# Kernel tuning notes

Measured on AMD Instinct MI355X. Metric: run time of the kernel, lower is better.

The kernel has to match this reference:

```python
import jax, jax.numpy as jnp
import numpy as np

NHID = 512
PROJ = 64          # fixed 64-dim projection from the source code
N_NODES = 16384
N_CLAIM = 4096
N_EVID = 8192
N_GRAPHS = 64


def setup_inputs() -> dict:
    key = jax.random.key(0)
    ks = jax.random.split(key, 10)
    x = jax.random.normal(ks[0], (N_NODES, NHID), dtype=jnp.float32)
    batch = jnp.sort(jax.random.randint(ks[1], (N_NODES,), 0, N_GRAPHS, dtype=jnp.int64))
    claim_index = jax.random.randint(ks[2], (N_CLAIM,), 0, N_NODES, dtype=jnp.int64)
    evidence_index = jax.random.randint(ks[3], (N_EVID,), 0, N_NODES, dtype=jnp.int64)
    # Linear params (PyTorch Linear: y = x @ W.T + b; store as [in, out] here)
    s_c = 1.0 / np.sqrt(NHID)
    Wc = jax.random.uniform(ks[4], (NHID, PROJ), jnp.float32, -s_c, s_c)
    bc = jax.random.uniform(ks[5], (PROJ,), jnp.float32, -s_c, s_c)
    We = jax.random.uniform(ks[6], (NHID, PROJ), jnp.float32, -s_c, s_c)
    be = jax.random.uniform(ks[7], (PROJ,), jnp.float32, -s_c, s_c)
    s_a = 1.0 / np.sqrt(4 * NHID)
    Wa = jax.random.uniform(ks[8], (4 * NHID, NHID), jnp.float32, -s_a, s_a)
    ba = jax.random.uniform(ks[9], (NHID,), jnp.float32, -s_a, s_a)
    return {"x": x, "batch": batch, "claim_index": claim_index,
            "evidence_index": evidence_index,
            "Wc": Wc, "bc": bc, "We": We, "be": be, "Wa": Wa, "ba": ba}


def reference(x, batch, claim_index, evidence_index, Wc, bc, We, be, Wa, ba):
    claim_batch = batch[claim_index]          # [Nc]
    evidence_batch = batch[evidence_index]    # [Ne]
    # block-diagonal mask: 0 where same graph, -inf otherwise
    same = claim_batch[:, None] == evidence_batch[None, :]
    mask = jnp.where(same, 0.0, -jnp.inf).astype(jnp.float32)  # [Nc, Ne]

    claim = x[claim_index]       # [Nc, nhid]
    evidence = x[evidence_index]  # [Ne, nhid]

    weight_c = claim @ Wc + bc    # [Nc, 64]
    weight_e = evidence @ We + be  # [Ne, 64]
    scores = weight_c @ weight_e.T + mask          # [Nc, Ne]
    attn = jax.nn.softmax(scores, axis=-1)
    claim_new = attn @ evidence                    # [Nc, nhid]

    a = jnp.concatenate([claim, claim_new, claim - claim_new, claim * claim_new], axis=-1)
    a = a @ Wa + ba               # [Nc, nhid]

    # global_mean_pool over claim_batch
    seg_sum = jax.ops.segment_sum(a, claim_batch, num_segments=N_GRAPHS)
    counts = jax.ops.segment_sum(jnp.ones((a.shape[0],), a.dtype), claim_batch,
                                 num_segments=N_GRAPHS)
    res = seg_sum / jnp.maximum(counts, 1.0)[:, None]  # [B, nhid]
    return res
```

## Files before the change

kernel.cpp:

```cpp
#include <hip/hip_runtime.h>
#include <hip/hip_bf16.h>

#define NHID 512
#define PROJ 64
#define NC 4096
#define NEV 8192
#define NG 64
#define NCMAX 128
#define NE_CAP 256
#define DSLICES 4
#define DW 128

typedef __attribute__((ext_vector_type(8))) short s16x8;
typedef __attribute__((ext_vector_type(8))) unsigned short u16x8;
typedef __attribute__((ext_vector_type(4))) float f32x4;

#define P_S_STRIDE 264
#define P_S_BYTES  (NCMAX * P_S_STRIDE * 2)
#define REGB_OFF   P_S_BYTES
#define WE_S_STRIDE 72
#define WC_S_OFF   (REGB_OFF + NE_CAP * WE_S_STRIDE * 2)
#define CN_S_STRIDE 132
#define MISC_OFF   (REGB_OFF + P_S_BYTES)
#define SMEM_BYTES (MISC_OFF + 1536)

static __device__ __forceinline__ unsigned short f2b(float f) {
  union { __hip_bfloat16 h; unsigned short u; } v;
  v.h = __float2bfloat16(f);
  return v.u;
}

template <int NPT>
__device__ __forceinline__ void compact_pairs(
    const int* __restrict__ batch, const int* __restrict__ idx, int g,
    int* __restrict__ off_out, int* __restrict__ cnt_out, int2* __restrict__ pairs) {
  __shared__ int wtot[4], wless[4];
  int t = threadIdx.x, lane = t & 63, w = t >> 6;
  int vals[NPT], nid[NPT];
  int base_i = t * NPT;
  int eq = 0, less = 0;
#pragma unroll
  for (int j = 0; j < NPT; j++) {
    int node = idx[base_i + j];
    int v = batch[node];
    vals[j] = v;
    nid[j] = node;
    eq += (v == g) ? 1 : 0;
    less += (v < g) ? 1 : 0;
  }
  int s = eq;
#pragma unroll
  for (int off = 1; off < 64; off <<= 1) {
    int o = __shfl_up(s, off);
    if (lane >= off) s += o;
  }
  int ls = less;
#pragma unroll
  for (int off = 32; off; off >>= 1) ls += __shfl_xor(ls, off);
  if (lane == 63) wtot[w] = s;
  if (lane == 0) wless[w] = ls;
  __syncthreads();
  int wbase = 0;
#pragma unroll
  for (int k = 0; k < 4; k++)
    if (k < w) wbase += wtot[k];
  int base = wless[0] + wless[1] + wless[2] + wless[3];
  int pos = base + wbase + (s - eq);
#pragma unroll
  for (int j = 0; j < NPT; j++) {
    if (vals[j] == g) pairs[pos++] = make_int2(base_i + j, nid[j]);
  }
  if (t == 255) {
    cnt_out[g] = wbase + s;
    off_out[g] = base;
  }
}

__global__ __launch_bounds__(256) void k_front(
    const float* __restrict__ Wc, const float* __restrict__ We,
    unsigned short* __restrict__ WcT, unsigned short* __restrict__ WeT,
    const int* __restrict__ batch, const int* __restrict__ cidx,
    const int* __restrict__ eidx, int* __restrict__ c_off, int* __restrict__ c_cnt,
    int2* __restrict__ c_pair, int* __restrict__ e_off, int* __restrict__ e_cnt,
    int2* __restrict__ e_pair) {
  int b = blockIdx.x;
  if (b < 16) {
    __shared__ float ts[64][65];
    const float* src = (b < 8) ? Wc : We;
    unsigned short* dst = (b < 8) ? WcT : WeT;
    int k0 = (b & 7) * 64;
    int t = threadIdx.x;
    int c = t & 63, r0 = t >> 6;
#pragma unroll
    for (int p = 0; p < 16; p++) {
      int r = r0 * 16 + p;
      ts[r][c] = src[(size_t)(k0 + r) * 64 + c];
    }
    __syncthreads();
    int n = t >> 2, q = t & 3;
    unsigned short tmp[16];
#pragma unroll
    for (int j = 0; j < 16; j++) tmp[j] = f2b(ts[q * 16 + j][n]);
    u16x8* dp = (u16x8*)(dst + (size_t)n * NHID + k0 + q * 16);
    dp[0] = *(u16x8*)tmp;
    dp[1] = *(u16x8*)(tmp + 8);
  } else if (b < 80) {
    compact_pairs<NC / 256>(batch, cidx, b - 16, c_off, c_cnt, c_pair);
  } else {
    compact_pairs<NEV / 256>(batch, eidx, b - 80, e_off, e_cnt, e_pair);
  }
}

__global__ __launch_bounds__(256) void k_proj(
    const float* __restrict__ x, const int* __restrict__ cidx,
    const int* __restrict__ eidx, const unsigned short* __restrict__ WcT,
    const unsigned short* __restrict__ WeT, const float* __restrict__ bc,
    const float* __restrict__ be, const float* __restrict__ Wa,
    unsigned short* __restrict__ WaT, unsigned short* __restrict__ wcp,
    unsigned short* __restrict__ wep) {
  __shared__ __align__(16) char sm[64 * 65 * 4];
  int b = blockIdx.x;
  int t = threadIdx.x;
  if (b >= 768) {
    int tb = b - 768;
    float(*ts)[65] = (float(*)[65])sm;
    int k0 = (tb >> 3) * 64, n0 = (tb & 7) * 64;
    int c = t & 63, r0 = t >> 6;
#pragma unroll
    for (int p = 0; p < 16; p++) {
      int r = r0 * 16 + p;
      ts[r][c] = Wa[(size_t)(k0 + r) * NHID + n0 + c];
    }
    __syncthreads();
    int n = t >> 2, q = t & 3;
    unsigned short tmp[16];
#pragma unroll
    for (int j = 0; j < 16; j++) tmp[j] = f2b(ts[q * 16 + j][n]);
    u16x8* dp = (u16x8*)(WaT + (size_t)(n0 + n) * (4 * NHID) + k0 + q * 16);
    dp[0] = *(u16x8*)tmp;
    dp[1] = *(u16x8*)(tmp + 8);
    return;
  }
  float(*red)[16][64] = (float(*)[16][64])sm;
  const int* idx; const unsigned short* WT; const float* bias;
  unsigned short* out; int base;
  if (b < NC / 16) { idx = cidx; WT = WcT; bias = bc; out = wcp; base = b * 16; }
  else             { idx = eidx; WT = WeT; bias = be; out = wep; base = (b - NC / 16) * 16; }
  int lane = t & 63, kh = t >> 6;
  int ln = lane & 15, kb = lane >> 4;
  const float* xr = x + (size_t)idx[base + ln] * NHID + kh * 128;
  const unsigned short* wb = WT + kh * 128;
  f32x4 acc[4];
#pragma unroll
  for (int nt = 0; nt < 4; nt++) acc[nt] = (f32x4){0.f, 0.f, 0.f, 0.f};
#pragma unroll
  for (int kt = 0; kt < 4; kt++) {
    int k0 = kt * 32 + kb * 8;
    float4 p0 = *(const float4*)(xr + k0);
    float4 p1 = *(const float4*)(xr + k0 + 4);
    s16x8 a;
    a[0] = (short)f2b(p0.x); a[1] = (short)f2b(p0.y);
    a[2] = (short)f2b(p0.z); a[3] = (short)f2b(p0.w);
    a[4] = (short)f2b(p1.x); a[5] = (short)f2b(p1.y);
    a[6] = (short)f2b(p1.z); a[7] = (short)f2b(p1.w);
#pragma unroll
    for (int nt = 0; nt < 4; nt++) {
      s16x8 bf = *(const s16x8*)(wb + (size_t)(nt * 16 + ln) * NHID + k0);
      acc[nt] = __builtin_amdgcn_mfma_f32_16x16x32_bf16(a, bf, acc[nt], 0, 0, 0);
    }
  }
#pragma unroll
  for (int nt = 0; nt < 4; nt++)
#pragma unroll
    for (int r = 0; r < 4; r++)
      red[kh][kb * 4 + r][nt * 16 + ln] = acc[nt][r];
  __syncthreads();
  for (int i = t; i < 512; i += 256) {
    int row = i >> 5, cp = i & 31;
    int c0 = cp * 2;
    float v0 = red[0][row][c0] + red[1][row][c0] + red[2][row][c0] + red[3][row][c0] + bias[c0];
    float v1 = red[0][row][c0 + 1] + red[1][row][c0 + 1] + red[2][row][c0 + 1] + red[3][row][c0 + 1] + bias[c0 + 1];
    unsigned int pk = (unsigned)f2b(v0) | ((unsigned)f2b(v1) << 16);
    *(unsigned int*)(out + (size_t)(base + row) * PROJ + c0) = pk;
  }
}

__global__ __launch_bounds__(512, 2) void k_attn(
    const float* __restrict__ x, const unsigned short* __restrict__ wcp,
    const unsigned short* __restrict__ wep, const int* __restrict__ c_off,
    const int* __restrict__ c_cnt, const int2* __restrict__ c_pair,
    const int* __restrict__ e_off, const int* __restrict__ e_cnt,
    const int2* __restrict__ e_pair, unsigned short* __restrict__ mcb) {
  __shared__ __align__(16) char smem[SMEM_BYTES];
  unsigned short* P_s  = (unsigned short*)(smem);
  unsigned short* we_s = (unsigned short*)(smem + REGB_OFF);
  unsigned short* wc_s = (unsigned short*)(smem + WC_S_OFF);
  unsigned short* evT  = (unsigned short*)(smem + REGB_OFF);
  unsigned int*   evT32 = (unsigned int*)(smem + REGB_OFF);
  float*          cn_s = (float*)(smem + REGB_OFF);
  float*          pp   = (float*)(smem);
  int* ev_id = (int*)(smem + MISC_OFF);
  int* cl_id = (int*)(smem + MISC_OFF + 1024);

  int g = blockIdx.x >> 2;
  int ds = blockIdx.x & 3;
  int dsbase = ds * DW;
  int t = threadIdx.x, lane = t & 63, w = t >> 6;
  int ln = lane & 15, kb = lane >> 4;

  int ne = min(e_cnt[g], NE_CAP);
  int eoff = e_off[g];
  int ccnt_full = c_cnt[g];
  int nloc = min(ccnt_full, NCMAX);
  int coff = c_off[g];
  if (nloc <= 0) {
    int q = t >> 7, d = t & 127;
    mcb[(size_t)g * 4 * NHID + q * NHID + dsbase + d] = 0;
    return;
  }
  int KT = (ne + 31) >> 5;
  int NT = KT * 2;

  for (int e = t; e < NE_CAP; e += 512)
    ev_id[e] = (e < ne) ? e_pair[eoff + e].y : 0;
  if (t < NCMAX) cl_id[t] = (t < nloc) ? c_pair[coff + t].y : 0;
  {
    int q = t & 7, er = t >> 3;
    for (int base_ = 0; base_ < NE_CAP; base_ += 64) {
      int e = base_ + er;
      u16x8 v = (u16x8){0, 0, 0, 0, 0, 0, 0, 0};
      if (e < ne) v = *(const u16x8*)(wep + (size_t)e_pair[eoff + e].x * PROJ + q * 8);
      *(u16x8*)(we_s + e * WE_S_STRIDE + q * 8) = v;
    }
    for (int base_ = 0; base_ < NCMAX; base_ += 64) {
      int c = base_ + er;
      u16x8 v = (u16x8){0, 0, 0, 0, 0, 0, 0, 0};
      if (c < nloc) v = *(const u16x8*)(wcp + (size_t)c_pair[coff + c].x * PROJ + q * 8);
      *(u16x8*)(wc_s + c * WE_S_STRIDE + q * 8) = v;
    }
  }
  __syncthreads();

  float4 eva[8], evb[8];
#pragma unroll
  for (int it = 0; it < 8; it++) {
    int idx2 = it * 512 + t;
    int ep = idx2 & 127;
    int dq = idx2 >> 7;
    int d0 = dq * 4;
    int e0 = ep * 2;
    eva[it] = make_float4(0.f, 0.f, 0.f, 0.f);
    evb[it] = make_float4(0.f, 0.f, 0.f, 0.f);
    if (e0 < ne)     eva[it] = *(const float4*)(x + (size_t)ev_id[e0] * NHID + dsbase + d0);
    if (e0 + 1 < ne) evb[it] = *(const float4*)(x + (size_t)ev_id[e0 + 1] * NHID + dsbase + d0);
  }

  {
    f32x4 sa[16];
#pragma unroll
    for (int i = 0; i < 16; i++) sa[i] = (f32x4){0.f, 0.f, 0.f, 0.f};
    const unsigned short* arow = wc_s + ((w << 4) + ln) * WE_S_STRIDE;
#pragma unroll
    for (int ks = 0; ks < 2; ks++) {
      s16x8 af = *(const s16x8*)(arow + ks * 32 + kb * 8);
#pragma unroll
      for (int nt = 0; nt < 16; nt++) {
        if (nt < NT) {
          s16x8 bf = *(const s16x8*)(we_s + (nt * 16 + ln) * WE_S_STRIDE + ks * 32 + kb * 8);
          sa[nt] = __builtin_amdgcn_mfma_f32_16x16x32_bf16(af, bf, sa[nt], 0, 0, 0);
        }
      }
    }
#pragma unroll
    for (int r = 0; r < 4; r++) {
      int claim = (w << 4) + (kb << 2) + r;
      float mx = -1e30f;
#pragma unroll
      for (int nt = 0; nt < 16; nt++) {
        if (nt < NT) {
          float v = sa[nt][r];
          v = (nt * 16 + ln < ne) ? v : -1e30f;
          sa[nt][r] = v;
          mx = fmaxf(mx, v);
        }
      }
      mx = fmaxf(mx, __shfl_xor(mx, 1));
      mx = fmaxf(mx, __shfl_xor(mx, 2));
      mx = fmaxf(mx, __shfl_xor(mx, 4));
      mx = fmaxf(mx, __shfl_xor(mx, 8));
      float sum = 0.f;
#pragma unroll
      for (int nt = 0; nt < 16; nt++) {
        if (nt < NT) {
          float p = __expf(sa[nt][r] - mx);
          sa[nt][r] = p;
          sum += p;
        }
      }
      sum += __shfl_xor(sum, 1);
      sum += __shfl_xor(sum, 2);
      sum += __shfl_xor(sum, 4);
      sum += __shfl_xor(sum, 8);
      float inv = 1.f / sum;
#pragma unroll
      for (int nt = 0; nt < 16; nt++) {
        if (nt < NT)
          P_s[claim * P_S_STRIDE + nt * 16 + ln] = f2b(sa[nt][r] * inv);
      }
    }
  }
  __syncthreads();

#pragma unroll
  for (int it = 0; it < 8; it++) {
    int idx2 = it * 512 + t;
    int ep = idx2 & 127;
    int dq = idx2 >> 7;
    int d0 = dq * 4;
    float4 va = eva[it], vb = evb[it];
    evT32[(d0 + 0) * (P_S_STRIDE / 2) + ep] = (unsigned)f2b(va.x) | ((unsigned)f2b(vb.x) << 16);
    evT32[(d0 + 1) * (P_S_STRIDE / 2) + ep] = (unsigned)f2b(va.y) | ((unsigned)f2b(vb.y) << 16);
    evT32[(d0 + 2) * (P_S_STRIDE / 2) + ep] = (unsigned)f2b(va.z) | ((unsigned)f2b(vb.z) << 16);
    evT32[(d0 + 3) * (P_S_STRIDE / 2) + ep] = (unsigned)f2b(va.w) | ((unsigned)f2b(vb.w) << 16);
  }
  __syncthreads();

  int dq4 = (t & 31) * 4;
  int mg = t >> 5;
  float4 cl_r[8];
#pragma unroll
  for (int mi = 0; mi < 8; mi++) {
    int m = mg + mi * 16;
    cl_r[mi] = make_float4(0.f, 0.f, 0.f, 0.f);
    if (m < nloc)
      cl_r[mi] = *(const float4*)(x + (size_t)cl_id[m] * NHID + dsbase + dq4);
  }

  int mw = w >> 1, nw = w & 1;
  int m0 = mw * 32, n0 = nw * 64;
  f32x4 pc[8];
#pragma unroll
  for (int i = 0; i < 8; i++) pc[i] = (f32x4){0.f, 0.f, 0.f, 0.f};
  {
    const unsigned short* prow0 = P_s + (m0 + ln) * P_S_STRIDE + kb * 8;
    const unsigned short* prow1 = prow0 + 16 * P_S_STRIDE;
#pragma unroll
    for (int kt = 0; kt < 8; kt++) {
      if (kt < KT) {
        int k0 = kt * 32;
        s16x8 a0 = *(const s16x8*)(prow0 + k0);
        s16x8 a1 = *(const s16x8*)(prow1 + k0);
#pragma unroll
        for (int nt = 0; nt < 4; nt++) {
          s16x8 bf = *(const s16x8*)(evT + (n0 + nt * 16 + ln) * P_S_STRIDE + k0 + kb * 8);
          pc[nt]     = __builtin_amdgcn_mfma_f32_16x16x32_bf16(a0, bf, pc[nt], 0, 0, 0);
          pc[4 + nt] = __builtin_amdgcn_mfma_f32_16x16x32_bf16(a1, bf, pc[4 + nt], 0, 0, 0);
        }
      }
    }
  }
  __syncthreads();

#pragma unroll
  for (int mi = 0; mi < 2; mi++) {
#pragma unroll
    for (int nt = 0; nt < 4; nt++) {
      f32x4 v = pc[mi * 4 + nt];
#pragma unroll
      for (int r = 0; r < 4; r++)
        cn_s[(m0 + mi * 16 + (kb << 2) + r) * CN_S_STRIDE + n0 + nt * 16 + ln] = v[r];
    }
  }
  __syncthreads();

  {
    float4 scl = make_float4(0.f, 0.f, 0.f, 0.f);
    float4 scn = make_float4(0.f, 0.f, 0.f, 0.f);
    float4 spr = make_float4(0.f, 0.f, 0.f, 0.f);
#pragma unroll
    for (int mi = 0; mi < 8; mi++) {
      int m = mg + mi * 16;
      if (m < nloc) {
        float4 cl = cl_r[mi];
        float4 cn = *(const float4*)(cn_s + m * CN_S_STRIDE + dq4);
        scl.x += cl.x; scl.y += cl.y; scl.z += cl.z; scl.w += cl.w;
        scn.x += cn.x; scn.y += cn.y; scn.z += cn.z; scn.w += cn.w;
        spr.x += cl.x * cn.x; spr.y += cl.y * cn.y;
        spr.z += cl.z * cn.z; spr.w += cl.w * cn.w;
      }
    }
    *(float4*)(pp + mg * 128 + dq4) = scl;
    *(float4*)(pp + 2048 + mg * 128 + dq4) = scn;
    *(float4*)(pp + 4096 + mg * 128 + dq4) = spr;
  }
  __syncthreads();

  {
    int q = t >> 7, d = t & 127;
    float inv = 1.f / (float)max(ccnt_full, 1);
    float v = 0.f;
    if (q == 0) {
#pragma unroll
      for (int mg2 = 0; mg2 < 16; mg2++) v += pp[mg2 * 128 + d];
    } else if (q == 1) {
#pragma unroll
      for (int mg2 = 0; mg2 < 16; mg2++) v += pp[2048 + mg2 * 128 + d];
    } else if (q == 2) {
#pragma unroll
      for (int mg2 = 0; mg2 < 16; mg2++) v += pp[mg2 * 128 + d] - pp[2048 + mg2 * 128 + d];
    } else {
#pragma unroll
      for (int mg2 = 0; mg2 < 16; mg2++) v += pp[4096 + mg2 * 128 + d];
    }
    mcb[(size_t)g * 4 * NHID + q * NHID + dsbase + d] = f2b(v * inv);
  }
}

__global__ __launch_bounds__(512) void k_out(
    const unsigned short* __restrict__ mc, const unsigned short* __restrict__ WaT,
    const float* __restrict__ ba, float* __restrict__ out) {
  __shared__ float red[2][64][16];
  int n0 = blockIdx.x * 16;
  int t = threadIdx.x, lane = t & 63, wv = t >> 6;
  int mh = wv & 3, kh = wv >> 2;
  int ln = lane & 15, kb = lane >> 4;
  f32x4 acc = (f32x4){0.f, 0.f, 0.f, 0.f};
  const unsigned short* arow = mc + (size_t)(mh * 16 + ln) * (4 * NHID) + kh * 1024;
  const unsigned short* wcol = WaT + (size_t)(n0 + ln) * (4 * NHID) + kh * 1024;
#pragma unroll 4
  for (int kt = 0; kt < 32; kt++) {
    int k0 = kt * 32 + kb * 8;
    s16x8 af = *(const s16x8*)(arow + k0);
    s16x8 bf = *(const s16x8*)(wcol + k0);
    acc = __builtin_amdgcn_mfma_f32_16x16x32_bf16(af, bf, acc, 0, 0, 0);
  }
#pragma unroll
  for (int r = 0; r < 4; r++)
    red[kh][mh * 16 + kb * 4 + r][ln] = acc[r];
  __syncthreads();
  for (int i = t; i < 1024; i += 512) {
    int row = i >> 4, col = i & 15;
    out[(size_t)row * NHID + n0 + col] = red[0][row][col] + red[1][row][col] + ba[n0 + col];
  }
}

extern "C" void kernel_launch(void* const* d_in, const int* in_sizes, int n_in,
                              void* d_out, int out_size, void* d_ws, size_t ws_size,
                              hipStream_t stream) {
  const float* x = (const float*)d_in[0];
  const int* batch = (const int*)d_in[1];
  const int* cidx = (const int*)d_in[2];
  const int* eidx = (const int*)d_in[3];
  const float* Wc = (const float*)d_in[4];
  const float* bc = (const float*)d_in[5];
  const float* We = (const float*)d_in[6];
  const float* be = (const float*)d_in[7];
  const float* Wa = (const float*)d_in[8];
  const float* ba = (const float*)d_in[9];
  float* out = (float*)d_out;

  char* w = (char*)d_ws;
  int* c_off = (int*)w;    w += NG * 4;
  int* c_cnt = (int*)w;    w += NG * 4;
  int* e_off = (int*)w;    w += NG * 4;
  int* e_cnt = (int*)w;    w += NG * 4;
  int2* c_pair = (int2*)w; w += (size_t)NC * 8;
  int2* e_pair = (int2*)w; w += (size_t)NEV * 8;
  unsigned short* wcp = (unsigned short*)w; w += (size_t)NC * PROJ * 2;
  unsigned short* wep = (unsigned short*)w; w += (size_t)NEV * PROJ * 2;
  unsigned short* WcT = (unsigned short*)w; w += (size_t)PROJ * NHID * 2;
  unsigned short* WeT = (unsigned short*)w; w += (size_t)PROJ * NHID * 2;
  unsigned short* WaT = (unsigned short*)w; w += (size_t)NHID * 4 * NHID * 2;
  unsigned short* mcb = (unsigned short*)w; w += (size_t)NG * 4 * NHID * 2;

  k_front<<<144, 256, 0, stream>>>(Wc, We, WcT, WeT, batch, cidx, eidx,
                                   c_off, c_cnt, c_pair, e_off, e_cnt, e_pair);
  k_proj<<<768 + 256, 256, 0, stream>>>(x, cidx, eidx, WcT, WeT, bc, be, Wa, WaT,
                                        wcp, wep);
  k_attn<<<NG * DSLICES, 512, 0, stream>>>(x, wcp, wep, c_off, c_cnt, c_pair,
                                           e_off, e_cnt, e_pair, mcb);
  k_out<<<32, 512, 0, stream>>>(mcb, WaT, ba, out);
}
```

Baseline: 58.30 us.

## Split attention kernel into per-graph score kernel and per-slice PV kernel

The fused attention kernel is split in two. A per-graph kernel computes the softmax probabilities once and writes them to a global bf16 buffer. A separate PV kernel, run per d-slice, reads those probabilities from global memory, so the score GEMM and softmax are no longer repeated for each of the four d-slices. The PV kernel uses less LDS, targets higher occupancy, and drops the cn_s staging buffer by reducing claim statistics with shuffles. In exchange it adds a kernel launch, a global round trip for the probabilities, and scalar rather than vectorized gathers of claim rows.

```diff
diff --git a/kernel.cpp b/kernel.cpp
--- a/kernel.cpp
+++ b/kernel.cpp
@@ -10,19 +10,13 @@
 #define NE_CAP 256
 #define DSLICES 4
 #define DW 128
+#define WE_S_STRIDE 72
+#define EV_STRIDE 264
+#define PG_STRIDE 256
 
 typedef __attribute__((ext_vector_type(8))) short s16x8;
 typedef __attribute__((ext_vector_type(8))) unsigned short u16x8;
 typedef __attribute__((ext_vector_type(4))) float f32x4;
-
-#define P_S_STRIDE 264
-#define P_S_BYTES  (NCMAX * P_S_STRIDE * 2)
-#define REGB_OFF   P_S_BYTES
-#define WE_S_STRIDE 72
-#define WC_S_OFF   (REGB_OFF + NE_CAP * WE_S_STRIDE * 2)
-#define CN_S_STRIDE 132
-#define MISC_OFF   (REGB_OFF + P_S_BYTES)
-#define SMEM_BYTES (MISC_OFF + 1536)
 
 static __device__ __forceinline__ unsigned short f2b(float f) {
   union { __hip_bfloat16 h; unsigned short u; } v;
@@ -185,22 +179,107 @@
   }
 }
 
-__global__ __launch_bounds__(512, 2) void k_attn(
-    const float* __restrict__ x, const unsigned short* __restrict__ wcp,
-    const unsigned short* __restrict__ wep, const int* __restrict__ c_off,
-    const int* __restrict__ c_cnt, const int2* __restrict__ c_pair,
-    const int* __restrict__ e_off, const int* __restrict__ e_cnt,
-    const int2* __restrict__ e_pair, unsigned short* __restrict__ mcb) {
-  __shared__ __align__(16) char smem[SMEM_BYTES];
-  unsigned short* P_s  = (unsigned short*)(smem);
-  unsigned short* we_s = (unsigned short*)(smem + REGB_OFF);
-  unsigned short* wc_s = (unsigned short*)(smem + WC_S_OFF);
-  unsigned short* evT  = (unsigned short*)(smem + REGB_OFF);
-  unsigned int*   evT32 = (unsigned int*)(smem + REGB_OFF);
-  float*          cn_s = (float*)(smem + REGB_OFF);
-  float*          pp   = (float*)(smem);
-  int* ev_id = (int*)(smem + MISC_OFF);
-  int* cl_id = (int*)(smem + MISC_OFF + 1024);
+__global__ __launch_bounds__(512) void k_score(
+    const unsigned short* __restrict__ wcp, const unsigned short* __restrict__ wep,
+    const int* __restrict__ c_off, const int* __restrict__ c_cnt,
+    const int2* __restrict__ c_pair, const int* __restrict__ e_off,
+    const int* __restrict__ e_cnt, const int2* __restrict__ e_pair,
+    unsigned short* __restrict__ P_g) {
+  __shared__ __align__(16) unsigned short we_s[NE_CAP * WE_S_STRIDE];
+  __shared__ __align__(16) unsigned short wc_s[NCMAX * WE_S_STRIDE];
+  int g = blockIdx.x;
+  int t = threadIdx.x, lane = t & 63, w = t >> 6;
+  int ln = lane & 15, kb = lane >> 4;
+  int ne = min(e_cnt[g], NE_CAP);
+  int eoff = e_off[g];
+  int nloc = min(c_cnt[g], NCMAX);
+  int coff = c_off[g];
+  if (nloc <= 0) return;
+  int KT = (ne + 31) >> 5;
+  int NT = KT * 2;
+  {
+    int q = t & 7, er = t >> 3;
+    for (int base_ = 0; base_ < NE_CAP; base_ += 64) {
+      int e = base_ + er;
+      u16x8 v = (u16x8){0, 0, 0, 0, 0, 0, 0, 0};
+      if (e < ne) v = *(const u16x8*)(wep + (size_t)e_pair[eoff + e].x * PROJ + q * 8);
+      *(u16x8*)(we_s + e * WE_S_STRIDE + q * 8) = v;
+    }
+    for (int base_ = 0; base_ < NCMAX; base_ += 64) {
+      int c = base_ + er;
+      u16x8 v = (u16x8){0, 0, 0, 0, 0, 0, 0, 0};
+      if (c < nloc) v = *(const u16x8*)(wcp + (size_t)c_pair[coff + c].x * PROJ + q * 8);
+      *(u16x8*)(wc_s + c * WE_S_STRIDE + q * 8) = v;
+    }
+  }
+  __syncthreads();
+  f32x4 sa[16];
+#pragma unroll
+  for (int i = 0; i < 16; i++) sa[i] = (f32x4){0.f, 0.f, 0.f, 0.f};
+  const unsigned short* arow = wc_s + ((w << 4) + ln) * WE_S_STRIDE;
+#pragma unroll
+  for (int ks = 0; ks < 2; ks++) {
+    s16x8 af = *(const s16x8*)(arow + ks * 32 + kb * 8);
+#pragma unroll
+    for (int nt = 0; nt < 16; nt++) {
+      if (nt < NT) {
+        s16x8 bf = *(const s16x8*)(we_s + (nt * 16 + ln) * WE_S_STRIDE + ks * 32 + kb * 8);
+        sa[nt] = __builtin_amdgcn_mfma_f32_16x16x32_bf16(af, bf, sa[nt], 0, 0, 0);
+      }
+    }
+  }
+#pragma unroll
+  for (int r = 0; r < 4; r++) {
+    int claim = (w << 4) + (kb << 2) + r;
+    float mx = -1e30f;
+#pragma unroll
+    for (int nt = 0; nt < 16; nt++) {
+      if (nt < NT) {
+        float v = sa[nt][r];
+        v = (nt * 16 + ln < ne) ? v : -1e30f;
+        sa[nt][r] = v;
+        mx = fmaxf(mx, v);
+      }
+    }
+    mx = fmaxf(mx, __shfl_xor(mx, 1));
+    mx = fmaxf(mx, __shfl_xor(mx, 2));
+    mx = fmaxf(mx, __shfl_xor(mx, 4));
+    mx = fmaxf(mx, __shfl_xor(mx, 8));
+    float sum = 0.f;
+#pragma unroll
+    for (int nt = 0; nt < 16; nt++) {
+      if (nt < NT) {
+        float p = __expf(sa[nt][r] - mx);
+        sa[nt][r] = p;
+        sum += p;
+      }
+    }
+    sum += __shfl_xor(sum, 1);
+    sum += __shfl_xor(sum, 2);
+    sum += __shfl_xor(sum, 4);
+    sum += __shfl_xor(sum, 8);
+    float inv = 1.f / sum;
+    if (claim < nloc) {
+      unsigned short* prow = P_g + (size_t)(coff + claim) * PG_STRIDE;
+#pragma unroll
+      for (int nt = 0; nt < 16; nt++) {
+        if (nt < NT) prow[nt * 16 + ln] = f2b(sa[nt][r] * inv);
+      }
+    }
+  }
+}
+
+__global__ __launch_bounds__(512, 4) void k_pv(
+    const float* __restrict__ x, const unsigned short* __restrict__ P_g,
+    const int* __restrict__ c_off, const int* __restrict__ c_cnt,
+    const int2* __restrict__ c_pair, const int* __restrict__ e_off,
+    const int* __restrict__ e_cnt, const int2* __restrict__ e_pair,
+    unsigned short* __restrict__ mcb) {
+  __shared__ __align__(16) unsigned short evT[DW * EV_STRIDE];
+  __shared__ float pp[4][3][DW];
+  __shared__ int ev_id[NE_CAP];
+  __shared__ int cl_id[NCMAX];
+  unsigned int* evT32 = (unsigned int*)evT;
 
   int g = blockIdx.x >> 2;
   int ds = blockIdx.x & 3;
@@ -219,29 +298,12 @@
     return;
   }
   int KT = (ne + 31) >> 5;
-  int NT = KT * 2;
 
   for (int e = t; e < NE_CAP; e += 512)
     ev_id[e] = (e < ne) ? e_pair[eoff + e].y : 0;
   if (t < NCMAX) cl_id[t] = (t < nloc) ? c_pair[coff + t].y : 0;
-  {
-    int q = t & 7, er = t >> 3;
-    for (int base_ = 0; base_ < NE_CAP; base_ += 64) {
-      int e = base_ + er;
-      u16x8 v = (u16x8){0, 0, 0, 0, 0, 0, 0, 0};
-      if (e < ne) v = *(const u16x8*)(wep + (size_t)e_pair[eoff + e].x * PROJ + q * 8);
-      *(u16x8*)(we_s + e * WE_S_STRIDE + q * 8) = v;
-    }
-    for (int base_ = 0; base_ < NCMAX; base_ += 64) {
-      int c = base_ + er;
-      u16x8 v = (u16x8){0, 0, 0, 0, 0, 0, 0, 0};
-      if (c < nloc) v = *(const u16x8*)(wcp + (size_t)c_pair[coff + c].x * PROJ + q * 8);
-      *(u16x8*)(wc_s + c * WE_S_STRIDE + q * 8) = v;
-    }
-  }
-  __syncthreads();
-
-  float4 eva[8], evb[8];
+  __syncthreads();
+
 #pragma unroll
   for (int it = 0; it < 8; it++) {
     int idx2 = it * 512 + t;
@@ -249,92 +311,16 @@
     int dq = idx2 >> 7;
     int d0 = dq * 4;
     int e0 = ep * 2;
-    eva[it] = make_float4(0.f, 0.f, 0.f, 0.f);
-    evb[it] = make_float4(0.f, 0.f, 0.f, 0.f);
-    if (e0 < ne)     eva[it] = *(const float4*)(x + (size_t)ev_id[e0] * NHID + dsbase + d0);
-    if (e0 + 1 < ne) evb[it] = *(const float4*)(x + (size_t)ev_id[e0 + 1] * NHID + dsbase + d0);
-  }
-
-  {
-    f32x4 sa[16];
-#pragma unroll
-    for (int i = 0; i < 16; i++) sa[i] = (f32x4){0.f, 0.f, 0.f, 0.f};
-    const unsigned short* arow = wc_s + ((w << 4) + ln) * WE_S_STRIDE;
-#pragma unroll
-    for (int ks = 0; ks < 2; ks++) {
-      s16x8 af = *(const s16x8*)(arow + ks * 32 + kb * 8);
-#pragma unroll
-      for (int nt = 0; nt < 16; nt++) {
-        if (nt < NT) {
-          s16x8 bf = *(const s16x8*)(we_s + (nt * 16 + ln) * WE_S_STRIDE + ks * 32 + kb * 8);
-          sa[nt] = __builtin_amdgcn_mfma_f32_16x16x32_bf16(af, bf, sa[nt], 0, 0, 0);
-        }
-      }
-    }
-#pragma unroll
-    for (int r = 0; r < 4; r++) {
-      int claim = (w << 4) + (kb << 2) + r;
-      float mx = -1e30f;
-#pragma unroll
-      for (int nt = 0; nt < 16; nt++) {
-        if (nt < NT) {
-          float v = sa[nt][r];
-          v = (nt * 16 + ln < ne) ? v : -1e30f;
-          sa[nt][r] = v;
-          mx = fmaxf(mx, v);
-        }
-      }
-      mx = fmaxf(mx, __shfl_xor(mx, 1));
-      mx = fmaxf(mx, __shfl_xor(mx, 2));
-      mx = fmaxf(mx, __shfl_xor(mx, 4));
-      mx = fmaxf(mx, __shfl_xor(mx, 8));
-      float sum = 0.f;
-#pragma unroll
-      for (int nt = 0; nt < 16; nt++) {
-        if (nt < NT) {
-          float p = __expf(sa[nt][r] - mx);
-          sa[nt][r] = p;
-          sum += p;
-        }
-      }
-      sum += __shfl_xor(sum, 1);
-      sum += __shfl_xor(sum, 2);
-      sum += __shfl_xor(sum, 4);
-      sum += __shfl_xor(sum, 8);
-      float inv = 1.f / sum;
-#pragma unroll
-      for (int nt = 0; nt < 16; nt++) {
-        if (nt < NT)
-          P_s[claim * P_S_STRIDE + nt * 16 + ln] = f2b(sa[nt][r] * inv);
-      }
-    }
-  }
-  __syncthreads();
-
-#pragma unroll
-  for (int it = 0; it < 8; it++) {
-    int idx2 = it * 512 + t;
-    int ep = idx2 & 127;
-    int dq = idx2 >> 7;
-    int d0 = dq * 4;
-    float4 va = eva[it], vb = evb[it];
-    evT32[(d0 + 0) * (P_S_STRIDE / 2) + ep] = (unsigned)f2b(va.x) | ((unsigned)f2b(vb.x) << 16);
-    evT32[(d0 + 1) * (P_S_STRIDE / 2) + ep] = (unsigned)f2b(va.y) | ((unsigned)f2b(vb.y) << 16);
-    evT32[(d0 + 2) * (P_S_STRIDE / 2) + ep] = (unsigned)f2b(va.z) | ((unsigned)f2b(vb.z) << 16);
-    evT32[(d0 + 3) * (P_S_STRIDE / 2) + ep] = (unsigned)f2b(va.w) | ((unsigned)f2b(vb.w) << 16);
-  }
-  __syncthreads();
-
-  int dq4 = (t & 31) * 4;
-  int mg = t >> 5;
-  float4 cl_r[8];
-#pragma unroll
-  for (int mi = 0; mi < 8; mi++) {
-    int m = mg + mi * 16;
-    cl_r[mi] = make_float4(0.f, 0.f, 0.f, 0.f);
-    if (m < nloc)
-      cl_r[mi] = *(const float4*)(x + (size_t)cl_id[m] * NHID + dsbase + dq4);
-  }
+    float4 va = make_float4(0.f, 0.f, 0.f, 0.f);
+    float4 vb = make_float4(0.f, 0.f, 0.f, 0.f);
+    if (e0 < ne)     va = *(const float4*)(x + (size_t)ev_id[e0] * NHID + dsbase + d0);
+    if (e0 + 1 < ne) vb = *(const float4*)(x + (size_t)ev_id[e0 + 1] * NHID + dsbase + d0);
+    evT32[(d0 + 0) * (EV_STRIDE / 2) + ep] = (unsigned)f2b(va.x) | ((unsigned)f2b(vb.x) << 16);
+    evT32[(d0 + 1) * (EV_STRIDE / 2) + ep] = (unsigned)f2b(va.y) | ((unsigned)f2b(vb.y) << 16);
+    evT32[(d0 + 2) * (EV_STRIDE / 2) + ep] = (unsigned)f2b(va.z) | ((unsigned)f2b(vb.z) << 16);
+    evT32[(d0 + 3) * (EV_STRIDE / 2) + ep] = (unsigned)f2b(va.w) | ((unsigned)f2b(vb.w) << 16);
+  }
+  __syncthreads();
 
   int mw = w >> 1, nw = w & 1;
   int m0 = mw * 32, n0 = nw * 64;
@@ -342,8 +328,8 @@
 #pragma unroll
   for (int i = 0; i < 8; i++) pc[i] = (f32x4){0.f, 0.f, 0.f, 0.f};
   {
-    const unsigned short* prow0 = P_s + (m0 + ln) * P_S_STRIDE + kb * 8;
-    const unsigned short* prow1 = prow0 + 16 * P_S_STRIDE;
+    const unsigned short* prow0 = P_g + (size_t)(coff + m0 + ln) * PG_STRIDE + kb * 8;
+    const unsigned short* prow1 = prow0 + 16 * PG_STRIDE;
 #pragma unroll
     for (int kt = 0; kt < 8; kt++) {
       if (kt < KT) {
@@ -352,65 +338,56 @@
         s16x8 a1 = *(const s16x8*)(prow1 + k0);
 #pragma unroll
         for (int nt = 0; nt < 4; nt++) {
-          s16x8 bf = *(const s16x8*)(evT + (n0 + nt * 16 + ln) * P_S_STRIDE + k0 + kb * 8);
+          s16x8 bf = *(const s16x8*)(evT + (n0 + nt * 16 + ln) * EV_STRIDE + k0 + kb * 8);
           pc[nt]     = __builtin_amdgcn_mfma_f32_16x16x32_bf16(a0, bf, pc[nt], 0, 0, 0);
           pc[4 + nt] = __builtin_amdgcn_mfma_f32_16x16x32_bf16(a1, bf, pc[4 + nt], 0, 0, 0);
         }
       }
     }
   }
-  __syncthreads();
-
-#pragma unroll
-  for (int mi = 0; mi < 2; mi++) {
-#pragma unroll
-    for (int nt = 0; nt < 4; nt++) {
+
+#pragma unroll
+  for (int nt = 0; nt < 4; nt++) {
+    int d = n0 + nt * 16 + ln;
+    float s_cl = 0.f, s_cn = 0.f, s_pr = 0.f;
+#pragma unroll
+    for (int mi = 0; mi < 2; mi++) {
       f32x4 v = pc[mi * 4 + nt];
 #pragma unroll
-      for (int r = 0; r < 4; r++)
-        cn_s[(m0 + mi * 16 + (kb << 2) + r) * CN_S_STRIDE + n0 + nt * 16 + ln] = v[r];
-    }
-  }
-  __syncthreads();
-
-  {
-    float4 scl = make_float4(0.f, 0.f, 0.f, 0.f);
-    float4 scn = make_float4(0.f, 0.f, 0.f, 0.f);
-    float4 spr = make_float4(0.f, 0.f, 0.f, 0.f);
-#pragma unroll
-    for (int mi = 0; mi < 8; mi++) {
-      int m = mg + mi * 16;
-      if (m < nloc) {
-        float4 cl = cl_r[mi];
-        float4 cn = *(const float4*)(cn_s + m * CN_S_STRIDE + dq4);
-        scl.x += cl.x; scl.y += cl.y; scl.z += cl.z; scl.w += cl.w;
-        scn.x += cn.x; scn.y += cn.y; scn.z += cn.z; scn.w += cn.w;
-        spr.x += cl.x * cn.x; spr.y += cl.y * cn.y;
-        spr.z += cl.z * cn.z; spr.w += cl.w * cn.w;
-      }
-    }
-    *(float4*)(pp + mg * 128 + dq4) = scl;
-    *(float4*)(pp + 2048 + mg * 128 + dq4) = scn;
-    *(float4*)(pp + 4096 + mg * 128 + dq4) = spr;
+      for (int r = 0; r < 4; r++) {
+        int m = m0 + mi * 16 + kb * 4 + r;
+        if (m < nloc) {
+          float cn = v[r];
+          float cl = x[(size_t)cl_id[m] * NHID + dsbase + d];
+          s_cl += cl; s_cn += cn; s_pr += cl * cn;
+        }
+      }
+    }
+    s_cl += __shfl_xor(s_cl, 16); s_cl += __shfl_xor(s_cl, 32);
+    s_cn += __shfl_xor(s_cn, 16); s_cn += __shfl_xor(s_cn, 32);
+    s_pr += __shfl_xor(s_pr, 16); s_pr += __shfl_xor(s_pr, 32);
+    if (kb == 0) {
+      pp[mw][0][d] = s_cl;
+      pp[mw][1][d] = s_cn;
+      pp[mw][2][d] = s_pr;
+    }
   }
   __syncthreads();
 
   {
     int q = t >> 7, d = t & 127;
     float inv = 1.f / (float)max(ccnt_full, 1);
-    float v = 0.f;
+    float v;
     if (q == 0) {
-#pragma unroll
-      for (int mg2 = 0; mg2 < 16; mg2++) v += pp[mg2 * 128 + d];
+      v = pp[0][0][d] + pp[1][0][d] + pp[2][0][d] + pp[3][0][d];
     } else if (q == 1) {
-#pragma unroll
-      for (int mg2 = 0; mg2 < 16; mg2++) v += pp[2048 + mg2 * 128 + d];
+      v = pp[0][1][d] + pp[1][1][d] + pp[2][1][d] + pp[3][1][d];
     } else if (q == 2) {
-#pragma unroll
-      for (int mg2 = 0; mg2 < 16; mg2++) v += pp[mg2 * 128 + d] - pp[2048 + mg2 * 128 + d];
+      float cl = pp[0][0][d] + pp[1][0][d] + pp[2][0][d] + pp[3][0][d];
+      float cn = pp[0][1][d] + pp[1][1][d] + pp[2][1][d] + pp[3][1][d];
+      v = cl - cn;
     } else {
-#pragma unroll
-      for (int mg2 = 0; mg2 < 16; mg2++) v += pp[4096 + mg2 * 128 + d];
+      v = pp[0][2][d] + pp[1][2][d] + pp[2][2][d] + pp[3][2][d];
     }
     mcb[(size_t)g * 4 * NHID + q * NHID + dsbase + d] = f2b(v * inv);
   }
@@ -472,12 +449,15 @@
   unsigned short* WeT = (unsigned short*)w; w += (size_t)PROJ * NHID * 2;
   unsigned short* WaT = (unsigned short*)w; w += (size_t)NHID * 4 * NHID * 2;
   unsigned short* mcb = (unsigned short*)w; w += (size_t)NG * 4 * NHID * 2;
+  unsigned short* P_g = (unsigned short*)w; w += (size_t)(NC + NCMAX) * PG_STRIDE * 2;
 
   k_front<<<144, 256, 0, stream>>>(Wc, We, WcT, WeT, batch, cidx, eidx,
                                    c_off, c_cnt, c_pair, e_off, e_cnt, e_pair);
   k_proj<<<768 + 256, 256, 0, stream>>>(x, cidx, eidx, WcT, WeT, bc, be, Wa, WaT,
                                         wcp, wep);
-  k_attn<<<NG * DSLICES, 512, 0, stream>>>(x, wcp, wep, c_off, c_cnt, c_pair,
-                                           e_off, e_cnt, e_pair, mcb);
+  k_score<<<NG, 512, 0, stream>>>(wcp, wep, c_off, c_cnt, c_pair,
+                                  e_off, e_cnt, e_pair, P_g);
+  k_pv<<<NG * DSLICES, 512, 0, stream>>>(x, P_g, c_off, c_cnt, c_pair,
+                                         e_off, e_cnt, e_pair, mcb);
   k_out<<<32, 512, 0, stream>>>(mcb, WaT, ba, out);
 }
```

Measured after the change: 68.85 us. 18.1% more time.

## Fuse output projection into attention kernel via atomic completion counter

Applied to the files above, without the earlier changes.

Removes the separate k_out launch. Every attention block increments a global counter when it finishes, and the first 32 blocks spin until all 256 blocks are done, then run the Wa projection and write the output. The counter is reset in k_front. This saves one kernel launch and its gap, but the tail now depends on a spin-wait. That is only safe if all 256 blocks can be resident at once (2 per CU is plausible on 256 CUs), and the 32 waiting blocks occupy slots while they spin.

```diff
diff --git a/kernel.cpp b/kernel.cpp
--- a/kernel.cpp
+++ b/kernel.cpp
@@ -82,8 +82,9 @@
     const int* __restrict__ batch, const int* __restrict__ cidx,
     const int* __restrict__ eidx, int* __restrict__ c_off, int* __restrict__ c_cnt,
     int2* __restrict__ c_pair, int* __restrict__ e_off, int* __restrict__ e_cnt,
-    int2* __restrict__ e_pair) {
+    int2* __restrict__ e_pair, int* __restrict__ ctr) {
   int b = blockIdx.x;
+  if (b == 0 && threadIdx.x == 0) *ctr = 0;
   if (b < 16) {
     __shared__ float ts[64][65];
     const float* src = (b < 8) ? Wc : We;
@@ -190,7 +191,9 @@
     const unsigned short* __restrict__ wep, const int* __restrict__ c_off,
     const int* __restrict__ c_cnt, const int2* __restrict__ c_pair,
     const int* __restrict__ e_off, const int* __restrict__ e_cnt,
-    const int2* __restrict__ e_pair, unsigned short* __restrict__ mcb) {
+    const int2* __restrict__ e_pair, unsigned short* __restrict__ mcb,
+    const unsigned short* __restrict__ WaT, const float* __restrict__ ba,
+    float* __restrict__ out, int* __restrict__ ctr) {
   __shared__ __align__(16) char smem[SMEM_BYTES];
   unsigned short* P_s  = (unsigned short*)(smem);
   unsigned short* we_s = (unsigned short*)(smem + REGB_OFF);
@@ -213,234 +216,242 @@
   int ccnt_full = c_cnt[g];
   int nloc = min(ccnt_full, NCMAX);
   int coff = c_off[g];
+
   if (nloc <= 0) {
     int q = t >> 7, d = t & 127;
     mcb[(size_t)g * 4 * NHID + q * NHID + dsbase + d] = 0;
-    return;
-  }
-  int KT = (ne + 31) >> 5;
-  int NT = KT * 2;
-
-  for (int e = t; e < NE_CAP; e += 512)
-    ev_id[e] = (e < ne) ? e_pair[eoff + e].y : 0;
-  if (t < NCMAX) cl_id[t] = (t < nloc) ? c_pair[coff + t].y : 0;
-  {
-    int q = t & 7, er = t >> 3;
-    for (int base_ = 0; base_ < NE_CAP; base_ += 64) {
-      int e = base_ + er;
-      u16x8 v = (u16x8){0, 0, 0, 0, 0, 0, 0, 0};
-      if (e < ne) v = *(const u16x8*)(wep + (size_t)e_pair[eoff + e].x * PROJ + q * 8);
-      *(u16x8*)(we_s + e * WE_S_STRIDE + q * 8) = v;
-    }
-    for (int base_ = 0; base_ < NCMAX; base_ += 64) {
-      int c = base_ + er;
-      u16x8 v = (u16x8){0, 0, 0, 0, 0, 0, 0, 0};
-      if (c < nloc) v = *(const u16x8*)(wcp + (size_t)c_pair[coff + c].x * PROJ + q * 8);
-      *(u16x8*)(wc_s + c * WE_S_STRIDE + q * 8) = v;
-    }
-  }
-  __syncthreads();
-
-  float4 eva[8], evb[8];
-#pragma unroll
-  for (int it = 0; it < 8; it++) {
-    int idx2 = it * 512 + t;
-    int ep = idx2 & 127;
-    int dq = idx2 >> 7;
-    int d0 = dq * 4;
-    int e0 = ep * 2;
-    eva[it] = make_float4(0.f, 0.f, 0.f, 0.f);
-    evb[it] = make_float4(0.f, 0.f, 0.f, 0.f);
-    if (e0 < ne)     eva[it] = *(const float4*)(x + (size_t)ev_id[e0] * NHID + dsbase + d0);
-    if (e0 + 1 < ne) evb[it] = *(const float4*)(x + (size_t)ev_id[e0 + 1] * NHID + dsbase + d0);
-  }
-
-  {
-    f32x4 sa[16];
-#pragma unroll
-    for (int i = 0; i < 16; i++) sa[i] = (f32x4){0.f, 0.f, 0.f, 0.f};
-    const unsigned short* arow = wc_s + ((w << 4) + ln) * WE_S_STRIDE;
-#pragma unroll
-    for (int ks = 0; ks < 2; ks++) {
-      s16x8 af = *(const s16x8*)(arow + ks * 32 + kb * 8);
-#pragma unroll
-      for (int nt = 0; nt < 16; nt++) {
-        if (nt < NT) {
-          s16x8 bf = *(const s16x8*)(we_s + (nt * 16 + ln) * WE_S_STRIDE + ks * 32 + kb * 8);
-          sa[nt] = __builtin_amdgcn_mfma_f32_16x16x32_bf16(af, bf, sa[nt], 0, 0, 0);
-        }
-      }
-    }
-#pragma unroll
-    for (int r = 0; r < 4; r++) {
-      int claim = (w << 4) + (kb << 2) + r;
-      float mx = -1e30f;
-#pragma unroll
-      for (int nt = 0; nt < 16; nt++) {
-        if (nt < NT) {
-          float v = sa[nt][r];
-          v = (nt * 16 + ln < ne) ? v : -1e30f;
-          sa[nt][r] = v;
-          mx = fmaxf(mx, v);
-        }
-      }
-      mx = fmaxf(mx, __shfl_xor(mx, 1));
-      mx = fmaxf(mx, __shfl_xor(mx, 2));
-      mx = fmaxf(mx, __shfl_xor(mx, 4));
-      mx = fmaxf(mx, __shfl_xor(mx, 8));
-      float sum = 0.f;
-#pragma unroll
-      for (int nt = 0; nt < 16; nt++) {
-        if (nt < NT) {
-          float p = __expf(sa[nt][r] - mx);
-          sa[nt][r] = p;
-          sum += p;
-        }
-      }
-      sum += __shfl_xor(sum, 1);
-      sum += __shfl_xor(sum, 2);
-      sum += __shfl_xor(sum, 4);
-      sum += __shfl_xor(sum, 8);
-      float inv = 1.f / sum;
-#pragma unroll
-      for (int nt = 0; nt < 16; nt++) {
-        if (nt < NT)
-          P_s[claim * P_S_STRIDE + nt * 16 + ln] = f2b(sa[nt][r] * inv);
-      }
-    }
-  }
-  __syncthreads();
-
-#pragma unroll
-  for (int it = 0; it < 8; it++) {
-    int idx2 = it * 512 + t;
-    int ep = idx2 & 127;
-    int dq = idx2 >> 7;
-    int d0 = dq * 4;
-    float4 va = eva[it], vb = evb[it];
-    evT32[(d0 + 0) * (P_S_STRIDE / 2) + ep] = (unsigned)f2b(va.x) | ((unsigned)f2b(vb.x) << 16);
-    evT32[(d0 + 1) * (P_S_STRIDE / 2) + ep] = (unsigned)f2b(va.y) | ((unsigned)f2b(vb.y) << 16);
-    evT32[(d0 + 2) * (P_S_STRIDE / 2) + ep] = (unsigned)f2b(va.z) | ((unsigned)f2b(vb.z) << 16);
-    evT32[(d0 + 3) * (P_S_STRIDE / 2) + ep] = (unsigned)f2b(va.w) | ((unsigned)f2b(vb.w) << 16);
-  }
-  __syncthreads();
-
-  int dq4 = (t & 31) * 4;
-  int mg = t >> 5;
-  float4 cl_r[8];
-#pragma unroll
-  for (int mi = 0; mi < 8; mi++) {
-    int m = mg + mi * 16;
-    cl_r[mi] = make_float4(0.f, 0.f, 0.f, 0.f);
-    if (m < nloc)
-      cl_r[mi] = *(const float4*)(x + (size_t)cl_id[m] * NHID + dsbase + dq4);
-  }
-
-  int mw = w >> 1, nw = w & 1;
-  int m0 = mw * 32, n0 = nw * 64;
-  f32x4 pc[8];
-#pragma unroll
-  for (int i = 0; i < 8; i++) pc[i] = (f32x4){0.f, 0.f, 0.f, 0.f};
-  {
-    const unsigned short* prow0 = P_s + (m0 + ln) * P_S_STRIDE + kb * 8;
-    const unsigned short* prow1 = prow0 + 16 * P_S_STRIDE;
-#pragma unroll
-    for (int kt = 0; kt < 8; kt++) {
-      if (kt < KT) {
-        int k0 = kt * 32;
-        s16x8 a0 = *(const s16x8*)(prow0 + k0);
-        s16x8 a1 = *(const s16x8*)(prow1 + k0);
-#pragma unroll
-        for (int nt = 0; nt < 4; nt++) {
-          s16x8 bf = *(const s16x8*)(evT + (n0 + nt * 16 + ln) * P_S_STRIDE + k0 + kb * 8);
-          pc[nt]     = __builtin_amdgcn_mfma_f32_16x16x32_bf16(a0, bf, pc[nt], 0, 0, 0);
-          pc[4 + nt] = __builtin_amdgcn_mfma_f32_16x16x32_bf16(a1, bf, pc[4 + nt], 0, 0, 0);
-        }
-      }
-    }
-  }
-  __syncthreads();
-
-#pragma unroll
-  for (int mi = 0; mi < 2; mi++) {
-#pragma unroll
-    for (int nt = 0; nt < 4; nt++) {
-      f32x4 v = pc[mi * 4 + nt];
-#pragma unroll
-      for (int r = 0; r < 4; r++)
-        cn_s[(m0 + mi * 16 + (kb << 2) + r) * CN_S_STRIDE + n0 + nt * 16 + ln] = v[r];
-    }
-  }
-  __syncthreads();
-
-  {
-    float4 scl = make_float4(0.f, 0.f, 0.f, 0.f);
-    float4 scn = make_float4(0.f, 0.f, 0.f, 0.f);
-    float4 spr = make_float4(0.f, 0.f, 0.f, 0.f);
+  } else {
+    int KT = (ne + 31) >> 5;
+    int NT = KT * 2;
+
+    for (int e = t; e < NE_CAP; e += 512)
+      ev_id[e] = (e < ne) ? e_pair[eoff + e].y : 0;
+    if (t < NCMAX) cl_id[t] = (t < nloc) ? c_pair[coff + t].y : 0;
+    {
+      int q = t & 7, er = t >> 3;
+      for (int base_ = 0; base_ < NE_CAP; base_ += 64) {
+        int e = base_ + er;
+        u16x8 v = (u16x8){0, 0, 0, 0, 0, 0, 0, 0};
+        if (e < ne) v = *(const u16x8*)(wep + (size_t)e_pair[eoff + e].x * PROJ + q * 8);
+        *(u16x8*)(we_s + e * WE_S_STRIDE + q * 8) = v;
+      }
+      for (int base_ = 0; base_ < NCMAX; base_ += 64) {
+        int c = base_ + er;
+        u16x8 v = (u16x8){0, 0, 0, 0, 0, 0, 0, 0};
+        if (c < nloc) v = *(const u16x8*)(wcp + (size_t)c_pair[coff + c].x * PROJ + q * 8);
+        *(u16x8*)(wc_s + c * WE_S_STRIDE + q * 8) = v;
+      }
+    }
+    __syncthreads();
+
+    float4 eva[8], evb[8];
+#pragma unroll
+    for (int it = 0; it < 8; it++) {
+      int idx2 = it * 512 + t;
+      int ep = idx2 & 127;
+      int dq = idx2 >> 7;
+      int d0 = dq * 4;
+      int e0 = ep * 2;
+      eva[it] = make_float4(0.f, 0.f, 0.f, 0.f);
+      evb[it] = make_float4(0.f, 0.f, 0.f, 0.f);
+      if (e0 < ne)     eva[it] = *(const float4*)(x + (size_t)ev_id[e0] * NHID + dsbase + d0);
+      if (e0 + 1 < ne) evb[it] = *(const float4*)(x + (size_t)ev_id[e0 + 1] * NHID + dsbase + d0);
+    }
+
+    {
+      f32x4 sa[16];
+#pragma unroll
+      for (int i = 0; i < 16; i++) sa[i] = (f32x4){0.f, 0.f, 0.f, 0.f};
+      const unsigned short* arow = wc_s + ((w << 4) + ln) * WE_S_STRIDE;
+#pragma unroll
+      for (int ks = 0; ks < 2; ks++) {
+        s16x8 af = *(const s16x8*)(arow + ks * 32 + kb * 8);
+#pragma unroll
+        for (int nt = 0; nt < 16; nt++) {
+          if (nt < NT) {
+            s16x8 bf = *(const s16x8*)(we_s + (nt * 16 + ln) * WE_S_STRIDE + ks * 32 + kb * 8);
+            sa[nt] = __builtin_amdgcn_mfma_f32_16x16x32_bf16(af, bf, sa[nt], 0, 0, 0);
+          }
+        }
+      }
+#pragma unroll
+      for (int r = 0; r < 4; r++) {
+        int claim = (w << 4) + (kb << 2) + r;
+        float mx = -1e30f;
+#pragma unroll
+        for (int nt = 0; nt < 16; nt++) {
+          if (nt < NT) {
+            float v = sa[nt][r];
+            v = (nt * 16 + ln < ne) ? v : -1e30f;
+            sa[nt][r] = v;
+            mx = fmaxf(mx, v);
+          }
+        }
+        mx = fmaxf(mx, __shfl_xor(mx, 1));
+        mx = fmaxf(mx, __shfl_xor(mx, 2));
+        mx = fmaxf(mx, __shfl_xor(mx, 4));
+        mx = fmaxf(mx, __shfl_xor(mx, 8));
+        float sum = 0.f;
+#pragma unroll
+        for (int nt = 0; nt < 16; nt++) {
+          if (nt < NT) {
+            float p = __expf(sa[nt][r] - mx);
+            sa[nt][r] = p;
+            sum += p;
+          }
+        }
+        sum += __shfl_xor(sum, 1);
+        sum += __shfl_xor(sum, 2);
+        sum += __shfl_xor(sum, 4);
+        sum += __shfl_xor(sum, 8);
+        float inv = 1.f / sum;
+#pragma unroll
+        for (int nt = 0; nt < 16; nt++) {
+          if (nt < NT)
+            P_s[claim * P_S_STRIDE + nt * 16 + ln] = f2b(sa[nt][r] * inv);
+        }
+      }
+    }
+    __syncthreads();
+
+#pragma unroll
+    for (int it = 0; it < 8; it++) {
+      int idx2 = it * 512 + t;
+      int ep = idx2 & 127;
+      int dq = idx2 >> 7;
+      int d0 = dq * 4;
+      float4 va = eva[it], vb = evb[it];
+      evT32[(d0 + 0) * (P_S_STRIDE / 2) + ep] = (unsigned)f2b(va.x) | ((unsigned)f2b(vb.x) << 16);
+      evT32[(d0 + 1) * (P_S_STRIDE / 2) + ep] = (unsigned)f2b(va.y) | ((unsigned)f2b(vb.y) << 16);
+      evT32[(d0 + 2) * (P_S_STRIDE / 2) + ep] = (unsigned)f2b(va.z) | ((unsigned)f2b(vb.z) << 16);
+      evT32[(d0 + 3) * (P_S_STRIDE / 2) + ep] = (unsigned)f2b(va.w) | ((unsigned)f2b(vb.w) << 16);
+    }
+    __syncthreads();
+
+    int dq4 = (t & 31) * 4;
+    int mg = t >> 5;
+    float4 cl_r[8];
 #pragma unroll
     for (int mi = 0; mi < 8; mi++) {
       int m = mg + mi * 16;
-      if (m < nloc) {
-        float4 cl = cl_r[mi];
-        float4 cn = *(const float4*)(cn_s + m * CN_S_STRIDE + dq4);
-        scl.x += cl.x; scl.y += cl.y; scl.z += cl.z; scl.w += cl.w;
-        scn.x += cn.x; scn.y += cn.y; scn.z += cn.z; scn.w += cn.w;
-        spr.x += cl.x * cn.x; spr.y += cl.y * cn.y;
-        spr.z += cl.z * cn.z; spr.w += cl.w * cn.w;
-      }
-    }
-    *(float4*)(pp + mg * 128 + dq4) = scl;
-    *(float4*)(pp + 2048 + mg * 128 + dq4) = scn;
-    *(float4*)(pp + 4096 + mg * 128 + dq4) = spr;
-  }
+      cl_r[mi] = make_float4(0.f, 0.f, 0.f, 0.f);
+      if (m < nloc)
+        cl_r[mi] = *(const float4*)(x + (size_t)cl_id[m] * NHID + dsbase + dq4);
+    }
+
+    int mw = w >> 1, nw = w & 1;
+    int m0 = mw * 32, n0 = nw * 64;
+    f32x4 pc[8];
+#pragma unroll
+    for (int i = 0; i < 8; i++) pc[i] = (f32x4){0.f, 0.f, 0.f, 0.f};
+    {
+      const unsigned short* prow0 = P_s + (m0 + ln) * P_S_STRIDE + kb * 8;
+      const unsigned short* prow1 = prow0 + 16 * P_S_STRIDE;
+#pragma unroll
+      for (int kt = 0; kt < 8; kt++) {
+        if (kt < KT) {
+          int k0 = kt * 32;
+          s16x8 a0 = *(const s16x8*)(prow0 + k0);
+          s16x8 a1 = *(const s16x8*)(prow1 + k0);
+#pragma unroll
+          for (int nt = 0; nt < 4; nt++) {
+            s16x8 bf = *(const s16x8*)(evT + (n0 + nt * 16 + ln) * P_S_STRIDE + k0 + kb * 8);
+            pc[nt]     = __builtin_amdgcn_mfma_f32_16x16x32_bf16(a0, bf, pc[nt], 0, 0, 0);
+            pc[4 + nt] = __builtin_amdgcn_mfma_f32_16x16x32_bf16(a1, bf, pc[4 + nt], 0, 0, 0);
+          }
+        }
+      }
+    }
+    __syncthreads();
+
+#pragma unroll
+    for (int mi = 0; mi < 2; mi++) {
+#pragma unroll
+      for (int nt = 0; nt < 4; nt++) {
+        f32x4 v = pc[mi * 4 + nt];
+#pragma unroll
+        for (int r = 0; r < 4; r++)
+          cn_s[(m0 + mi * 16 + (kb << 2) + r) * CN_S_STRIDE + n0 + nt * 16 + ln] = v[r];
+      }
+    }
+    __syncthreads();
+
+    {
+      float4 scl = make_float4(0.f, 0.f, 0.f, 0.f);
+      float4 scn = make_float4(0.f, 0.f, 0.f, 0.f);
+      float4 spr = make_float4(0.f, 0.f, 0.f, 0.f);
+#pragma unroll
+      for (int mi = 0; mi < 8; mi++) {
+        int m = mg + mi * 16;
+        if (m < nloc) {
+          float4 cl = cl_r[mi];
+          float4 cn = *(const float4*)(cn_s + m * CN_S_STRIDE + dq4);
+          scl.x += cl.x; scl.y += cl.y; scl.z += cl.z; scl.w += cl.w;
+          scn.x += cn.x; scn.y += cn.y; scn.z += cn.z; scn.w += cn.w;
+          spr.x += cl.x * cn.x; spr.y += cl.y * cn.y;
+          spr.z += cl.z * cn.z; spr.w += cl.w * cn.w;
+        }
+      }
+      *(float4*)(pp + mg * 128 + dq4) = scl;
+      *(float4*)(pp + 2048 + mg * 128 + dq4) = scn;
+      *(float4*)(pp + 4096 + mg * 128 + dq4) = spr;
+    }
+    __syncthreads();
+
+    {
+      int q = t >> 7, d = t & 127;
+      float inv = 1.f / (float)max(ccnt_full, 1);
+      float v = 0.f;
+      if (q == 0) {
+#pragma unroll
+        for (int mg2 = 0; mg2 < 16; mg2++) v += pp[mg2 * 128 + d];
+      } else if (q == 1) {
+#pragma unroll
+        for (int mg2 = 0; mg2 < 16; mg2++) v += pp[2048 + mg2 * 128 + d];
+      } else if (q == 2) {
+#pragma unroll
+        for (int mg2 = 0; mg2 < 16; mg2++) v += pp[mg2 * 128 + d] - pp[2048 + mg2 * 128 + d];
+      } else {
+#pragma unroll
+        for (int mg2 = 0; mg2 < 16; mg2++) v += pp[4096 + mg2 * 128 + d];
+      }
+      mcb[(size_t)g * 4 * NHID + q * NHID + dsbase + d] = f2b(v * inv);
+    }
+  }
+
   __syncthreads();
-
-  {
-    int q = t >> 7, d = t & 127;
-    float inv = 1.f / (float)max(ccnt_full, 1);
-    float v = 0.f;
-    if (q == 0) {
-#pragma unroll
-      for (int mg2 = 0; mg2 < 16; mg2++) v += pp[mg2 * 128 + d];
-    } else if (q == 1) {
-#pragma unroll
-      for (int mg2 = 0; mg2 < 16; mg2++) v += pp[2048 + mg2 * 128 + d];
-    } else if (q == 2) {
-#pragma unroll
-      for (int mg2 = 0; mg2 < 16; mg2++) v += pp[mg2 * 128 + d] - pp[2048 + mg2 * 128 + d];
-    } else {
-#pragma unroll
-      for (int mg2 = 0; mg2 < 16; mg2++) v += pp[4096 + mg2 * 128 + d];
-    }
-    mcb[(size_t)g * 4 * NHID + q * NHID + dsbase + d] = f2b(v * inv);
-  }
-}
-
-__global__ __launch_bounds__(512) void k_out(
-    const unsigned short* __restrict__ mc, const unsigned short* __restrict__ WaT,
-    const float* __restrict__ ba, float* __restrict__ out) {
-  __shared__ float red[2][64][16];
-  int n0 = blockIdx.x * 16;
-  int t = threadIdx.x, lane = t & 63, wv = t >> 6;
-  int mh = wv & 3, kh = wv >> 2;
-  int ln = lane & 15, kb = lane >> 4;
-  f32x4 acc = (f32x4){0.f, 0.f, 0.f, 0.f};
-  const unsigned short* arow = mc + (size_t)(mh * 16 + ln) * (4 * NHID) + kh * 1024;
-  const unsigned short* wcol = WaT + (size_t)(n0 + ln) * (4 * NHID) + kh * 1024;
+  if (t == 0) {
+    __threadfence();
+    atomicAdd(ctr, 1);
+  }
+
+  if (blockIdx.x < 32) {
+    if (t == 0) {
+      while (__hip_atomic_load(ctr, __ATOMIC_ACQUIRE, __HIP_MEMORY_SCOPE_AGENT) < 256)
+        __builtin_amdgcn_s_sleep(2);
+    }
+    __syncthreads();
+    float(*red)[64][16] = (float(*)[64][16])smem;
+    int n0 = blockIdx.x * 16;
+    int mh = w & 3, kh = w >> 2;
+    f32x4 acc = (f32x4){0.f, 0.f, 0.f, 0.f};
+    const unsigned short* arow = mcb + (size_t)(mh * 16 + ln) * (4 * NHID) + kh * 1024;
+    const unsigned short* wcol = WaT + (size_t)(n0 + ln) * (4 * NHID) + kh * 1024;
 #pragma unroll 4
-  for (int kt = 0; kt < 32; kt++) {
-    int k0 = kt * 32 + kb * 8;
-    s16x8 af = *(const s16x8*)(arow + k0);
-    s16x8 bf = *(const s16x8*)(wcol + k0);
-    acc = __builtin_amdgcn_mfma_f32_16x16x32_bf16(af, bf, acc, 0, 0, 0);
-  }
-#pragma unroll
-  for (int r = 0; r < 4; r++)
-    red[kh][mh * 16 + kb * 4 + r][ln] = acc[r];
-  __syncthreads();
-  for (int i = t; i < 1024; i += 512) {
-    int row = i >> 4, col = i & 15;
-    out[(size_t)row * NHID + n0 + col] = red[0][row][col] + red[1][row][col] + ba[n0 + col];
+    for (int kt = 0; kt < 32; kt++) {
+      int k0 = kt * 32 + kb * 8;
+      s16x8 af = *(const s16x8*)(arow + k0);
+      s16x8 bf = *(const s16x8*)(wcol + k0);
+      acc = __builtin_amdgcn_mfma_f32_16x16x32_bf16(af, bf, acc, 0, 0, 0);
+    }
+#pragma unroll
+    for (int r = 0; r < 4; r++)
+      red[kh][mh * 16 + kb * 4 + r][ln] = acc[r];
+    __syncthreads();
+    for (int i = t; i < 1024; i += 512) {
+      int row = i >> 4, col = i & 15;
+      out[(size_t)row * NHID + n0 + col] = red[0][row][col] + red[1][row][col] + ba[n0 + col];
+    }
   }
 }
 
@@ -464,6 +475,7 @@
   int* c_cnt = (int*)w;    w += NG * 4;
   int* e_off = (int*)w;    w += NG * 4;
   int* e_cnt = (int*)w;    w += NG * 4;
+  int* ctr = (int*)w;      w += 64;
   int2* c_pair = (int2*)w; w += (size_t)NC * 8;
   int2* e_pair = (int2*)w; w += (size_t)NEV * 8;
   unsigned short* wcp = (unsigned short*)w; w += (size_t)NC * PROJ * 2;
@@ -474,10 +486,10 @@
   unsigned short* mcb = (unsigned short*)w; w += (size_t)NG * 4 * NHID * 2;
 
   k_front<<<144, 256, 0, stream>>>(Wc, We, WcT, WeT, batch, cidx, eidx,
-                                   c_off, c_cnt, c_pair, e_off, e_cnt, e_pair);
+                                   c_off, c_cnt, c_pair, e_off, e_cnt, e_pair, ctr);
   k_proj<<<768 + 256, 256, 0, stream>>>(x, cidx, eidx, WcT, WeT, bc, be, Wa, WaT,
                                         wcp, wep);
   k_attn<<<NG * DSLICES, 512, 0, stream>>>(x, wcp, wep, c_off, c_cnt, c_pair,
-                                           e_off, e_cnt, e_pair, mcb);
-  k_out<<<32, 512, 0, stream>>>(mcb, WaT, ba, out);
-}
+                                           e_off, e_cnt, e_pair, mcb,
+                                           WaT, ba, out, ctr);
+}
```

After: 62.94 us. 8.0% more time.
